# Optimization experiments

Measured on AMD Instinct MI355X. Metric: run time of the kernel, lower is better.

The kernel has to match this reference:

```python
import jax, jax.numpy as jnp
import numpy as np

# ---- static config (matches init_kwargs) ----
B, SX, SY, SZ = 1, 64, 64, 64
W = 32            # HIDDEN_DIM
L = 4             # num_fourier_layers
M1 = M2 = M3 = 8  # fourier modes per axis
PX = PY = PZ = 8  # domain padding
ALPHA = 0.05      # leaky relu slope
OUTC = 6


def conv3d(x, w, pad):
    # x: (B,C,D,H,W), w: (O,I,kd,kh,kw)
    return jax.lax.conv_general_dilated(
        x, w, window_strides=(1, 1, 1), padding=[(pad, pad)] * 3,
        dimension_numbers=('NCDHW', 'OIDHW', 'NCDHW'))


def pad1(x):
    # periodic=(0,0,0) -> zero pad 1 on every spatial side (matches ZeroPad3d chain)
    return jnp.pad(x, ((0, 0), (0, 0), (1, 1), (1, 1), (1, 1)))


def basic_block(x, w1, w2):
    # BasicBlock3D_Periodic with use_shortcut=False
    out = jax.nn.leaky_relu(conv3d(pad1(x), w1, 0), ALPHA)
    return conv3d(pad1(out), w2, 0)


def spec_apply(xft_slice, w):
    # xft_slice: complex (B,C,d1,d2,d3); w: (2C,2C,5,5,5)
    re_im = jnp.concatenate([xft_slice.real, xft_slice.imag], axis=1)  # (B,2C,...)
    out = conv3d(re_im, w, 2)                                          # (B,2C,...)
    b, c2, d1, d2, d3 = out.shape
    out = out.reshape(b, c2 // 2, 2, d1, d2, d3)
    return jax.lax.complex(out[:, :, 0], out[:, :, 1])


def spectral_conv(x, ws):
    # ws: (8, 2W, 2W, 5, 5, 5); mode-limited per-octant conv in frequency space
    b, c, n, m, l = x.shape
    xft = jnp.fft.rfftn(x, axes=(-3, -2, -1))  # (b,c,n,m,l//2+1) complex
    out = jnp.zeros((b, c, n, m, l // 2 + 1), dtype=xft.dtype)
    octs = [
        (slice(None, M1),  slice(None, M2)),
        (slice(n - M1, None), slice(None, M2)),
        (slice(None, M1),  slice(m - M2, None)),
        (slice(n - M1, None), slice(m - M2, None)),
        (slice(M1, n - M1), slice(None, M2)),
        (slice(None, M1),  slice(M2, m - M2)),
        (slice(M1, n - M1), slice(m - M2, None)),
        (slice(n - M1, None), slice(M2, m - M2)),
    ]
    for i, (s1, s2) in enumerate(octs):
        out = out.at[:, :, s1, s2, :M3].set(spec_apply(xft[:, :, s1, s2, :M3], ws[i]))
    return jnp.fft.irfftn(out, s=(n, m, l), axes=(-3, -2, -1))


def setup_inputs() -> dict:
    key = jax.random.key(0)
    ks = jax.random.split(key, 16)
    f32 = jnp.float32
    d = {
        'yeex': jax.random.normal(ks[0], (B, SX, SY, SZ), f32),
        'yeey': jax.random.normal(ks[1], (B, SX, SY, SZ), f32),
        'yeez': jax.random.normal(ks[2], (B, SX, SY, SZ), f32),
        'fc0_w': jax.random.normal(ks[3], (6, W), f32) * 0.1,
        'fc0_b': jax.random.normal(ks[4], (W,), f32) * 0.01,
        'spec_w': jax.random.normal(ks[5], (L, 8, 2 * W, 2 * W, 5, 5, 5), f32) * 0.02,
        'blk_w1': jax.random.normal(ks[6], (L, W, W, 3, 3, 3), f32) * 0.05,
        'blk_w2': jax.random.normal(ks[7], (L, W, W, 3, 3, 3), f32) * 0.05,
        'fc1_w': jax.random.normal(ks[8], (W, 128), f32) * 0.05,
        'fc1_b': jax.random.normal(ks[9], (128,), f32) * 0.01,
        'fc2_w': jax.random.normal(ks[10], (128, OUTC), f32) * 0.05,
        'fc2_b': jax.random.normal(ks[11], (OUTC,), f32) * 0.01,
    }
    return d


def reference(yeex, yeey, yeez, fc0_w, fc0_b, spec_w, blk_w1, blk_w2,
              fc1_w, fc1_b, fc2_w, fc2_b):
    b, sx, sy, sz = yeez.shape
    # normalized coordinate grid (3 channels), as in standard FNO get_grid
    gx = jnp.broadcast_to(jnp.linspace(0., 1., sx, dtype=yeex.dtype)[None, :, None, None], (b, sx, sy, sz))
    gy = jnp.broadcast_to(jnp.linspace(0., 1., sy, dtype=yeex.dtype)[None, None, :, None], (b, sx, sy, sz))
    gz = jnp.broadcast_to(jnp.linspace(0., 1., sz, dtype=yeex.dtype)[None, None, None, :], (b, sx, sy, sz))
    inp = jnp.stack([yeex, yeey, yeez, gx, gy, gz], axis=-1)  # (b,sx,sy,sz,6)

    x = inp @ fc0_w + fc0_b                      # lift: (b,sx,sy,sz,W)
    x = jnp.transpose(x, (0, 4, 1, 2, 3))        # (b,W,sx,sy,sz)
    x = jnp.pad(x, ((0, 0), (0, 0), (0, PX), (0, PY), (0, PZ)))

    for i in range(L):
        x1 = spectral_conv(x, spec_w[i])
        x2 = basic_block(x, blk_w1[i], blk_w2[i])
        x = x1 + x2 + x
        if i < L - 1:
            x = jax.nn.leaky_relu(x, ALPHA)

    x = x[:, :, :sx, :sy, :sz]                   # crop domain padding
    x = jnp.transpose(x, (0, 2, 3, 4, 1))        # (b,sx,sy,sz,W)
    x = jax.nn.leaky_relu(x @ fc1_w + fc1_b, ALPHA)
    return x @ fc2_w + fc2_b                     # (b,sx,sy,sz,OUTC)
```

## Files before the change

kernel.cpp:

```cpp
#include <hip/hip_runtime.h>
#include <math.h>

#define NS 72
#define NS2 (NS*NS)
#define NS3 (NS*NS*NS)
#define MZ 8
#define LALPHA 0.05f
#define CSCALE (1.0f/256.0f)

typedef _Float16 f16x8 __attribute__((ext_vector_type(8)));
typedef _Float16 f16x4 __attribute__((ext_vector_type(4)));
typedef float f32x4 __attribute__((ext_vector_type(4)));

__device__ __forceinline__ float leakyf(float v){ return v > 0.f ? v : LALPHA*v; }

__constant__ int c_RX0[8] = {0,64,0,64, 8,0,8,64};
__constant__ int c_RNX[8] = {8,8,8,8, 56,8,56,8};
__constant__ int c_RY0[8] = {0,0,64,64, 0,8,64,8};
__constant__ int c_RNY[8] = {8,8,8,8, 8,56,8,56};
__constant__ int c_Bbase[8] = {0,1728,3456,5184, 6912,15552,24192,32832};
__constant__ int c_BY[8]    = {12,12,12,12, 12,60,12,60};

__global__ void k_tw(float2* tw){
  int t = threadIdx.x;
  if (t < NS){
    double th = (2.0*M_PI/72.0)*(double)t;
    tw[t] = make_float2((float)cos(th), (float)sin(th));
  }
}

__global__ void k_fc0(const float* __restrict__ yx, const float* __restrict__ yy,
                      const float* __restrict__ yz, const float* __restrict__ w,
                      const float* __restrict__ b, float* __restrict__ X){
  int idx = blockIdx.x*256 + threadIdx.x;
  int z = idx % NS; int t = idx / NS; int y = t % NS; t /= NS; int x = t % NS; int c = t / NS;
  float v = 0.f;
  if (x < 64 && y < 64 && z < 64){
    int p = (x*64 + y)*64 + z;
    float i0 = yx[p], i1 = yy[p], i2 = yz[p];
    float gx = (float)x*(1.f/63.f), gy = (float)y*(1.f/63.f), gz = (float)z*(1.f/63.f);
    v = b[c] + i0*w[0*32+c] + i1*w[1*32+c] + i2*w[2*32+c]
             + gx*w[3*32+c] + gy*w[4*32+c] + gz*w[5*32+c];
  }
  X[idx] = v;
}

__global__ void k_zdft(const float* __restrict__ X, float2* __restrict__ A, const float2* __restrict__ tw){
  __shared__ float2 stw[NS];
  int tid = threadIdx.x;
  if (tid < NS) stw[tid] = tw[tid];
  __syncthreads();
  int f = blockIdx.x*256 + tid;
  const float* row = X + (size_t)f*NS;
  float ar[MZ], ai[MZ]; int tk[MZ];
  #pragma unroll
  for (int k=0;k<MZ;k++){ ar[k]=0.f; ai[k]=0.f; tk[k]=0; }
  for (int z4=0; z4<NS; z4+=4){
    float4 v4 = *(const float4*)(row + z4);
    float vs[4] = {v4.x, v4.y, v4.z, v4.w};
    #pragma unroll
    for (int zz=0; zz<4; zz++){
      float v = vs[zz];
      #pragma unroll
      for (int k=0;k<MZ;k++){
        float2 w = stw[tk[k]];
        ar[k] += v*w.x;
        ai[k] -= v*w.y;
        tk[k] += k; if (tk[k] >= NS) tk[k] -= NS;
      }
    }
  }
  float2* o = A + (size_t)f*MZ;
  #pragma unroll
  for (int k=0;k<MZ;k++) o[k] = make_float2(ar[k], ai[k]);
}

__global__ void k_ydft(const float2* __restrict__ A, float2* __restrict__ B, const float2* __restrict__ tw){
  __shared__ float2 stw[NS];
  int tid = threadIdx.x;
  if (tid < NS) stw[tid] = tw[tid];
  __syncthreads();
  int f = blockIdx.x*256 + tid;
  int ky = f % NS; int cx = f / NS;
  const float2* in = A + (size_t)cx*NS*MZ;
  float ar[MZ], ai[MZ];
  #pragma unroll
  for (int k=0;k<MZ;k++){ ar[k]=0.f; ai[k]=0.f; }
  int t = 0;
  for (int y=0;y<NS;y++){
    float2 w = stw[t]; t += ky; if (t>=NS) t-=NS;
    const float2* iy = in + y*MZ;
    #pragma unroll
    for (int k=0;k<MZ;k++){
      float2 v = iy[k];
      ar[k] += v.x*w.x + v.y*w.y;
      ai[k] += v.y*w.x - v.x*w.y;
    }
  }
  float2* o = B + (size_t)f*MZ;
  #pragma unroll
  for (int k=0;k<MZ;k++) o[k] = make_float2(ar[k], ai[k]);
}

__global__ void k_xdftL(const float2* __restrict__ B, float2* __restrict__ C, const float2* __restrict__ tw){
  __shared__ float2 stw[NS];
  int tid = threadIdx.x;
  if (tid < NS) stw[tid] = tw[tid];
  __syncthreads();
  int t = blockIdx.x*256 + tid;
  int h = t & 1; int t2 = t >> 1;
  int c = t2 >> 11; int l = t2 & 2047;
  int kx, ky;
  if (l < 576){ ky = l & 7; kx = l >> 3; }
  else if (l < 1152){ int e = l - 576; ky = 64 + (e & 7); kx = e >> 3; }
  else { int e = l - 1152; int kyi = e >> 4; int kxi = e & 15;
         ky = 8 + kyi; kx = (kxi < 8) ? kxi : 56 + kxi; }
  int k0 = h*4;
  const float2* in = B + ((size_t)c*NS2 + ky)*MZ + k0;
  float ar[4], ai[4];
  #pragma unroll
  for (int k=0;k<4;k++){ ar[k]=0.f; ai[k]=0.f; }
  int tt = 0;
  for (int x=0;x<NS;x++){
    float2 w = stw[tt]; tt += kx; if (tt>=NS) tt-=NS;
    const float2* ix = in + (size_t)x*NS*MZ;
    #pragma unroll
    for (int k=0;k<4;k++){
      float2 v = ix[k];
      ar[k] += v.x*w.x + v.y*w.y;
      ai[k] += v.y*w.x - v.x*w.y;
    }
  }
  float2* o = C + (((size_t)c*NS + kx)*NS + ky)*MZ + k0;
  #pragma unroll
  for (int k=0;k<4;k++) o[k] = make_float2(ar[k], ai[k]);
}

__global__ void k_wpackh(const float* __restrict__ W, _Float16* __restrict__ Ah){
  int e = blockIdx.x*256 + threadIdx.x;
  int i = e & 63; int o = (e>>6) & 63;
  int t2 = e >> 12; int tap = t2 % 125; int r = t2 / 125;
  const float* wr = W + (size_t)r*64*64*125;
  Ah[e] = (_Float16)wr[((size_t)(o*64 + (i&1)*32 + (i>>1)))*125 + tap];
}

__global__ void k_cpackh(const float2* __restrict__ C, _Float16* __restrict__ Bg){
  int g = blockIdx.x*256 + threadIdx.x;
  int ci = g & 31; int elem = g >> 5;
  int r = 0;
  #pragma unroll
  for (int k=1;k<8;k++) if (elem >= c_Bbase[k]) r = k;
  int el = elem - c_Bbase[r];
  int BY = c_BY[r];
  int q3 = el % 12; int tt = el / 12; int q2 = tt % BY; int q1 = tt / BY;
  int kxr = q1-2, kyr = q2-2, kzr = q3-2;
  float2 v = make_float2(0.f,0.f);
  if ((unsigned)kxr < (unsigned)c_RNX[r] && (unsigned)kyr < (unsigned)c_RNY[r] && (unsigned)kzr < 8u){
    v = C[(((size_t)ci*NS + (c_RX0[r]+kxr))*NS + (c_RY0[r]+kyr))*MZ + kzr];
  }
  _Float16* o = Bg + (size_t)elem*64 + 2*ci;
  o[0] = (_Float16)(v.x*CSCALE);
  o[1] = (_Float16)(v.y*CSCALE);
}

__global__ __launch_bounds__(64) void k_freqmfma(const _Float16* __restrict__ Ah,
                                                 const _Float16* __restrict__ Bg,
                                                 float* __restrict__ Pp){
  int gb = blockIdx.x;
  int ks = gb >> 8; int b = gb & 255;
  int r, til;
  if (b < 32){ r = b>>3; til = b&7; }
  else       { r = 4 + (b-32)/56; til = (b-32)%56; }
  int BY = c_BY[r];
  int q1, q2base;
  if (r==5 || r==7){ q1 = 2 + til/7; q2base = 2 + (til%7)*8; }
  else             { q1 = 2 + til;   q2base = 2; }
  int lane = threadIdx.x;
  int l15 = lane & 15, kg = lane >> 4;
  int q2l = q2base + (l15>>3), q3l = 2 + (l15&7);
  const _Float16* Ar = Ah + (size_t)r*125*4096;
  const _Float16* Br = Bg + (size_t)c_Bbase[r]*64;
  int lb = q2l*12 + q3l;
  f32x4 acc[4][4];
  f32x4 zz = {0.f,0.f,0.f,0.f};
  #pragma unroll
  for (int m=0;m<4;m++)
    #pragma unroll
    for (int n=0;n<4;n++) acc[m][n] = zz;
  int t0 = ks*16;
  int t1 = t0+16 < 125 ? t0+16 : 125;
  for (int tt=t0; tt<t1; tt++){
    int td = tt/25; int rm = tt - td*25; int th = rm/5; int tz = rm - th*5;
    const _Float16* At = Ar + tt*4096;
    f16x8 a[4][2];
    #pragma unroll
    for (int mt=0;mt<4;mt++){
      a[mt][0] = *(const f16x8*)(At + (mt*16+l15)*64 + kg*8);
      a[mt][1] = *(const f16x8*)(At + (mt*16+l15)*64 + 32 + kg*8);
    }
    int ebase = (q1 + td - 2)*BY*12 + lb + (th-2)*12 + (tz-2);
    f16x8 bf[4][2];
    #pragma unroll
    for (int nt=0;nt<4;nt++){
      const _Float16* bp = Br + (size_t)(ebase + nt*24)*64 + kg*8;
      bf[nt][0] = *(const f16x8*)(bp);
      bf[nt][1] = *(const f16x8*)(bp + 32);
    }
    #pragma unroll
    for (int mt=0;mt<4;mt++)
      #pragma unroll
      for (int nt=0;nt<4;nt++){
        acc[mt][nt] = __builtin_amdgcn_mfma_f32_16x16x32_f16(a[mt][0], bf[nt][0], acc[mt][nt],0,0,0);
        acc[mt][nt] = __builtin_amdgcn_mfma_f32_16x16x32_f16(a[mt][1], bf[nt][1], acc[mt][nt],0,0,0);
      }
  }
  float* base = Pp + (((size_t)ks*256 + b)*64 + lane)*64;
  #pragma unroll
  for (int mt=0;mt<4;mt++)
    #pragma unroll
    for (int nt=0;nt<4;nt++)
      *(f32x4*)(base + mt*16 + nt*4) = acc[mt][nt];
}

__global__ void k_fred(const float* __restrict__ Pp, float* __restrict__ Df){
  int t = blockIdx.x*256 + threadIdx.x;
  int mtnt = t & 15; int lane = (t>>4) & 63; int b = t >> 10;
  int mt = mtnt >> 2, nt = mtnt & 3;
  int r, til;
  if (b < 32){ r = b>>3; til = b&7; }
  else       { r = 4 + (b-32)/56; til = (b-32)%56; }
  int x0 = c_RX0[r], y0 = c_RY0[r];
  int q1, q2base;
  if (r==5 || r==7){ q1 = 2 + til/7; q2base = 2 + (til%7)*8; }
  else             { q1 = 2 + til;   q2base = 2; }
  int l15 = lane & 15, kg = lane >> 4;
  int q2l = q2base + (l15>>3), q3l = 2 + (l15&7);
  f32x4 s = {0.f,0.f,0.f,0.f};
  #pragma unroll
  for (int ks=0;ks<8;ks++){
    s += *(const f32x4*)(Pp + (((size_t)ks*256 + b)*64 + lane)*64 + mtnt*4);
  }
  int kx = x0 + q1 - 2;
  int kz = q3l - 2;
  int ky = y0 + q2l + nt*2 - 2;
  #pragma unroll
  for (int rg=0;rg<4;rg++){
    int o = mt*16 + kg*4 + rg;
    int co = o >> 1, reim = o & 1;
    Df[((((size_t)co*NS + kx)*NS + ky)*MZ + kz)*2 + reim] = s[rg]*256.0f;
  }
}

__global__ void k_invx(const float2* __restrict__ D, float2* __restrict__ E, const float2* __restrict__ tw){
  __shared__ float2 stw[NS];
  int tid = threadIdx.x;
  if (tid < NS) stw[tid] = tw[tid];
  __syncthreads();
  int f = blockIdx.x*256 + tid;
  int ky = f / 2304; int rem = f - ky*2304;
  int c = rem / NS; int x = rem - c*NS;
  const float2* in = D + ((size_t)c*NS2 + ky)*MZ;
  float ar[MZ], ai[MZ];
  #pragma unroll
  for (int k=0;k<MZ;k++){ ar[k]=0.f; ai[k]=0.f; }
  if (ky >= 8 && ky < 64){
    int t = 0;
    for (int kx=0;kx<8;kx++){
      float2 w = stw[t]; t += x; if (t>=NS) t-=NS;
      const float2* ix = in + (size_t)kx*NS*MZ;
      #pragma unroll
      for (int k=0;k<MZ;k++){
        float2 v = ix[k];
        ar[k] += v.x*w.x - v.y*w.y;
        ai[k] += v.x*w.y + v.y*w.x;
      }
    }
    t = (64*x) % NS;
    for (int kx=64;kx<NS;kx++){
      float2 w = stw[t]; t += x; if (t>=NS) t-=NS;
      const float2* ix = in + (size_t)kx*NS*MZ;
      #pragma unroll
      for (int k=0;k<MZ;k++){
        float2 v = ix[k];
        ar[k] += v.x*w.x - v.y*w.y;
        ai[k] += v.x*w.y + v.y*w.x;
      }
    }
  } else {
    int t = 0;
    for (int kx=0;kx<NS;kx++){
      float2 w = stw[t]; t += x; if (t>=NS) t-=NS;
      const float2* ix = in + (size_t)kx*NS*MZ;
      #pragma unroll
      for (int k=0;k<MZ;k++){
        float2 v = ix[k];
        ar[k] += v.x*w.x - v.y*w.y;
        ai[k] += v.x*w.y + v.y*w.x;
      }
    }
  }
  float2* o = E + (((size_t)c*NS + x)*NS + ky)*MZ;
  #pragma unroll
  for (int k=0;k<MZ;k++) o[k] = make_float2(ar[k]*(1.f/72.f), ai[k]*(1.f/72.f));
}

__global__ void k_invyz(const float2* __restrict__ E, _Float16* __restrict__ X1h, const float2* __restrict__ tw){
  __shared__ float2 stw[NS];
  int tid = threadIdx.x;
  if (tid < NS) stw[tid] = tw[tid];
  __syncthreads();
  int f = blockIdx.x*256 + tid;
  int y = f % NS; int t2 = f / NS; int x = t2 % NS; int c = t2 / NS;
  const float2* in = E + ((size_t)c*NS + x)*NS*MZ;
  float ar[MZ], ai[MZ];
  #pragma unroll
  for (int k=0;k<MZ;k++){ ar[k]=0.f; ai[k]=0.f; }
  int t = 0;
  for (int ky=0;ky<NS;ky++){
    float2 w = stw[t]; t += y; if (t>=NS) t-=NS;
    const float2* ik = in + ky*MZ;
    #pragma unroll
    for (int k=0;k<MZ;k++){
      float2 v = ik[k];
      ar[k] += v.x*w.x - v.y*w.y;
      ai[k] += v.x*w.y + v.y*w.x;
    }
  }
  const float scale = 1.f/(72.f*72.f);
  _Float16* o = X1h + (size_t)f*NS;
  int tk[MZ];
  #pragma unroll
  for (int k=0;k<MZ;k++) tk[k]=0;
  for (int z4=0; z4<NS; z4+=4){
    f16x4 hv;
    #pragma unroll
    for (int zz=0; zz<4; zz++){
      float acc = ar[0];
      #pragma unroll
      for (int k=1;k<MZ;k++){
        float2 w = stw[tk[k]];
        acc += 2.f*(ar[k]*w.x - ai[k]*w.y);
        tk[k] += k; if (tk[k] >= NS) tk[k] -= NS;
      }
      hv[zz] = (_Float16)(acc*scale);
    }
    *(f16x4*)(o + z4) = hv;
  }
}


__global__ void k_wcvt2(const float* __restrict__ w1, const float* __restrict__ w2,
                        _Float16* __restrict__ WhA, _Float16* __restrict__ WhB){
  int e = blockIdx.x*256 + threadIdx.x;
  int h = e >= 27648; int e2 = e - (h ? 27648 : 0);
  int tap = e2 >> 10; int co = (e2>>5)&31; int ci = e2&31;
  const float* w = h ? w2 : w1;
  _Float16* o = h ? WhB : WhA;
  o[e2] = (_Float16)w[(co*32+ci)*27 + tap];
}

__global__ void k_cvt16(const float* __restrict__ Xf, _Float16* __restrict__ Xg){
  int b = blockIdx.x;
  int tid = threadIdx.x;
  if (b >= 1458){
    _Float16* g = (b==1458) ? (Xg - 4096) : (Xg + (size_t)NS3*32);
    f16x8 zz = {0,0,0,0,0,0,0,0};
    f16x8* gp = (f16x8*)g;
    gp[tid] = zz; gp[tid+256] = zz;
    return;
  }
  int p = b*256 + tid;
  f16x8 o0,o1,o2,o3;
  #pragma unroll
  for (int c=0;c<8;c++){
    o0[c] = (_Float16)Xf[(size_t)c*NS3 + p];
    o1[c] = (_Float16)Xf[(size_t)(c+8)*NS3 + p];
    o2[c] = (_Float16)Xf[(size_t)(c+16)*NS3 + p];
    o3[c] = (_Float16)Xf[(size_t)(c+24)*NS3 + p];
  }
  f16x8* op = (f16x8*)(Xg + (size_t)p*32);
  op[0]=o0; op[1]=o1; op[2]=o2; op[3]=o3;
}

__global__ void k_zgH(_Float16* __restrict__ Hg){
  int e = blockIdx.x*256 + threadIdx.x;
  _Float16* g = (e < 512) ? (Hg - 4096 + e*8)
                          : (Hg + (size_t)NS3*32 + (size_t)(e-512)*8);
  f16x8 zz = {0,0,0,0,0,0,0,0};
  *(f16x8*)g = zz;
}

__global__ __launch_bounds__(256) void k_convm(const _Float16* __restrict__ Xg,
    const _Float16* __restrict__ Wh, float* __restrict__ OUT, _Float16* __restrict__ OUTH,
    const _Float16* __restrict__ X1h, const _Float16* __restrict__ XresH,
    int mode2, int do_leaky){
  int tid = threadIdx.x;
  int orig = blockIdx.x;
  int xcd = orig & 7, loc = orig >> 3;
  int wg = (xcd < 2 ? xcd*183 : 366 + (xcd-2)*182) + loc;
  int j = wg*4 + (tid>>6);
  int slab = j/81, nb = j - slab*81;
  int q0 = nb*64;
  int lane = tid & 63;
  int l15 = lane & 15, kg = lane >> 4;
  f32x4 acc[2][4];
  f32x4 zz = {0.f,0.f,0.f,0.f};
  #pragma unroll
  for (int a=0;a<2;a++)
    #pragma unroll
    for (int b=0;b<4;b++) acc[a][b] = zz;
  for (int dx=0; dx<3; dx++){
    int xx = slab + dx - 1;
    if ((unsigned)xx >= 72u) continue;
    const _Float16* Xrow = Xg + ((size_t)xx*5184 + q0)*32;
    #pragma unroll
    for (int t9=0; t9<9; t9++){
      int tap = dx*9 + t9;
      int off = ((t9/3)-1)*72 + (t9%3) - 1;
      f16x8 a0 = *(const f16x8*)(Wh + ((tap*32 + l15)*32 + kg*8));
      f16x8 a1 = *(const f16x8*)(Wh + ((tap*32 + 16 + l15)*32 + kg*8));
      const _Float16* bbase = Xrow + (off + l15)*32 + kg*8;
      f16x8 b0 = *(const f16x8*)(bbase);
      f16x8 b1 = *(const f16x8*)(bbase + 512);
      f16x8 b2 = *(const f16x8*)(bbase + 1024);
      f16x8 b3 = *(const f16x8*)(bbase + 1536);
      acc[0][0] = __builtin_amdgcn_mfma_f32_16x16x32_f16(a0,b0,acc[0][0],0,0,0);
      acc[0][1] = __builtin_amdgcn_mfma_f32_16x16x32_f16(a0,b1,acc[0][1],0,0,0);
      acc[0][2] = __builtin_amdgcn_mfma_f32_16x16x32_f16(a0,b2,acc[0][2],0,0,0);
      acc[0][3] = __builtin_amdgcn_mfma_f32_16x16x32_f16(a0,b3,acc[0][3],0,0,0);
      acc[1][0] = __builtin_amdgcn_mfma_f32_16x16x32_f16(a1,b0,acc[1][0],0,0,0);
      acc[1][1] = __builtin_amdgcn_mfma_f32_16x16x32_f16(a1,b1,acc[1][1],0,0,0);
      acc[1][2] = __builtin_amdgcn_mfma_f32_16x16x32_f16(a1,b2,acc[1][2],0,0,0);
      acc[1][3] = __builtin_amdgcn_mfma_f32_16x16x32_f16(a1,b3,acc[1][3],0,0,0);
    }
  }
  if (mode2){
    #pragma unroll
    for (int nt=0; nt<4; nt++){
      int q = q0 + nt*16 + l15;
      int y = q/72, z = q - y*72;
      bool edge = (y==0)||(y==71)||(z==0)||(z==71);
      #pragma unroll
      for (int c2=0;c2<2;c2++){
        #pragma unroll
        for (int r=0;r<4;r++){
          int co = c2*16 + kg*4 + r;
          size_t idx = (size_t)co*NS3 + (size_t)slab*5184 + q;
          float v = acc[c2][nt][r];
          if (!edge){
            v += (float)X1h[idx] + (float)XresH[((size_t)slab*5184 + q)*32 + co];
            if (do_leaky) v = leakyf(v);
          }
          OUT[idx] = v;
        }
      }
    }
  } else {
    #pragma unroll
    for (int nt=0; nt<4; nt++){
      int q = q0 + nt*16 + l15;
      int y = q/72, z = q - y*72;
      bool edge = (y==0)||(y==71)||(z==0)||(z==71);
      _Float16* hp = OUTH + ((size_t)slab*5184 + q)*32 + kg*4;
      #pragma unroll
      for (int c2=0;c2<2;c2++){
        f32x4 av = acc[c2][nt];
        f16x4 hv;
        #pragma unroll
        for (int r=0;r<4;r++){
          float v = av[r];
          if (!edge) v = leakyf(v);
          hv[r] = (_Float16)v;
        }
        *(f16x4*)(hp + c2*16) = hv;
      }
    }
  }
}

__global__ void k_corrH(_Float16* __restrict__ H, const _Float16* __restrict__ Xg,
                        const _Float16* __restrict__ Wh){
  int t = blockIdx.x*256 + threadIdx.x;
  int co = t & 31; int t2 = t >> 5;
  int e = t2 % 284; int x = t2 / 284;
  int y, z;
  if (e < 72){ y = 0; z = e; }
  else if (e < 144){ y = 71; z = e - 72; }
  else if (e < 214){ z = 0; y = e - 143; }
  else { z = 71; y = e - 213; }
  int q = y*72 + z;
  float corr = 0.f;
  for (int tap=0; tap<27; tap++){
    int dx = tap/9, rr = tap%9, dy = rr/3, dz = rr%3;
    int xx = x + dx - 1;
    if ((unsigned)xx >= 72u) continue;
    int yy = y + dy - 1, zz = z + dz - 1;
    if ((unsigned)yy < 72u && (unsigned)zz < 72u) continue;
    int lin = (xx*5184 + q + (dy-1)*72 + (dz-1))*32;
    const _Float16* V = Xg + lin;
    const _Float16* Wr = Wh + (tap*32 + co)*32;
    float s = 0.f;
    #pragma unroll
    for (int ci=0; ci<32; ci++) s += (float)V[ci]*(float)Wr[ci];
    corr += s;
  }
  size_t idx = ((size_t)x*5184 + q)*32 + co;
  float v = (float)H[idx] - corr;
  v = leakyf(v);
  H[idx] = (_Float16)v;
}

__global__ void k_corr(float* __restrict__ OUT, const _Float16* __restrict__ Xg,
                       const _Float16* __restrict__ Wh, const _Float16* __restrict__ X1h,
                       const _Float16* __restrict__ XresH, int mode2, int do_leaky){
  int t = blockIdx.x*256 + threadIdx.x;
  int co = t & 31; int t2 = t >> 5;
  int e = t2 % 284; int x = t2 / 284;
  int y, z;
  if (e < 72){ y = 0; z = e; }
  else if (e < 144){ y = 71; z = e - 72; }
  else if (e < 214){ z = 0; y = e - 143; }
  else { z = 71; y = e - 213; }
  int q = y*72 + z;
  float corr = 0.f;
  for (int tap=0; tap<27; tap++){
    int dx = tap/9, rr = tap%9, dy = rr/3, dz = rr%3;
    int xx = x + dx - 1;
    if ((unsigned)xx >= 72u) continue;
    int yy = y + dy - 1, zz = z + dz - 1;
    if ((unsigned)yy < 72u && (unsigned)zz < 72u) continue;
    int lin = (xx*5184 + q + (dy-1)*72 + (dz-1))*32;
    const _Float16* V = Xg + lin;
    const _Float16* Wr = Wh + (tap*32 + co)*32;
    float s = 0.f;
    #pragma unroll
    for (int ci=0; ci<32; ci++) s += (float)V[ci]*(float)Wr[ci];
    corr += s;
  }
  size_t idx = (size_t)co*NS3 + (size_t)x*5184 + q;
  float v = OUT[idx] - corr;
  if (mode2) v += (float)X1h[idx] + (float)XresH[((size_t)x*5184 + q)*32 + co];
  if (do_leaky) v = leakyf(v);
  OUT[idx] = v;
}

__global__ void k_head(const float* __restrict__ X, const float* __restrict__ w1, const float* __restrict__ b1,
                       const float* __restrict__ w2, const float* __restrict__ b2, float* __restrict__ out){
  __shared__ float s1t[32*128];
  __shared__ float sb1[128];
  __shared__ float s2[128*6];
  __shared__ float sb2[6];
  int tid = threadIdx.x;
  for (int e=tid;e<4096;e+=256){ int j=e>>5, c=e&31; s1t[e]=w1[c*128+j]; }
  if (tid<128) sb1[tid]=b1[tid];
  for (int e=tid;e<768;e+=256) s2[e]=w2[e];
  if (tid<6) sb2[tid]=b2[tid];
  __syncthreads();
  int p0 = blockIdx.x*256 + tid;
  float xin[2][32];
  float acc[2][6];
  #pragma unroll
  for (int vv=0; vv<2; vv++){
    int p = p0 + vv*131072;
    int z = p % 64; int t = p / 64; int y = t % 64; int x = t / 64;
    size_t q = ((size_t)x*NS + y)*NS + z;
    #pragma unroll
    for (int c=0;c<32;c++) xin[vv][c] = X[(size_t)c*NS3 + q];
    #pragma unroll
    for (int o=0;o<6;o++) acc[vv][o]=sb2[o];
  }
  for (int j=0;j<128;j++){
    const float4* wj = (const float4*)(s1t + j*32);
    float h0 = sb1[j], h1 = h0;
    #pragma unroll
    for (int c4=0;c4<8;c4++){
      float4 w = wj[c4];
      h0 += xin[0][c4*4+0]*w.x + xin[0][c4*4+1]*w.y + xin[0][c4*4+2]*w.z + xin[0][c4*4+3]*w.w;
      h1 += xin[1][c4*4+0]*w.x + xin[1][c4*4+1]*w.y + xin[1][c4*4+2]*w.z + xin[1][c4*4+3]*w.w;
    }
    h0 = leakyf(h0); h1 = leakyf(h1);
    const float* s2j = s2 + j*6;
    #pragma unroll
    for (int o=0;o<6;o++){
      float wv = s2j[o];
      acc[0][o] += h0*wv;
      acc[1][o] += h1*wv;
    }
  }
  #pragma unroll
  for (int vv=0; vv<2; vv++){
    float* O = out + (size_t)(p0 + vv*131072)*6;
    #pragma unroll
    for (int o=0;o<6;o++) O[o]=acc[vv][o];
  }
}

extern "C" void kernel_launch(void* const* d_in, const int* in_sizes, int n_in,
                              void* d_out, int out_size, void* d_ws, size_t ws_size,
                              hipStream_t stream) {
  const float* yeex = (const float*)d_in[0];
  const float* yeey = (const float*)d_in[1];
  const float* yeez = (const float*)d_in[2];
  const float* fc0w = (const float*)d_in[3];
  const float* fc0b = (const float*)d_in[4];
  const float* specw= (const float*)d_in[5];
  const float* bw1  = (const float*)d_in[6];
  const float* bw2  = (const float*)d_in[7];
  const float* fc1w = (const float*)d_in[8];
  const float* fc1b = (const float*)d_in[9];
  const float* fc2w = (const float*)d_in[10];
  const float* fc2b = (const float*)d_in[11];
  float* out = (float*)d_out;
  float* ws  = (float*)d_ws;

  float*  P0 = ws;
  float*  X1s = ws + 11943936;
  float*  P2 = ws + 23887872;
  float2* A  = (float2*)(ws + 35831808);
  float2* B  = (float2*)(ws + 41140224);
  float2* Cf = (float2*)(ws + 46448640);
  float2* Df = (float2*)(ws + 51757056);
  float2* TW = (float2*)(ws + 57065472);
  _Float16* Ah = (_Float16*)A;
  _Float16* Bg = (_Float16*)B;
  float*    Pp = X1s;
  _Float16* X1h = (_Float16*)X1s;
  _Float16* XhG = (_Float16*)(ws + 35831808) + 4096;
  _Float16* HhG = (_Float16*)(ws + 41807872) + 4096;
  _Float16* WhA = (_Float16*)(ws + 47783936);
  _Float16* WhB = (_Float16*)(ws + 47797760);

  float* curX = P0; float* curY = P2;

  k_tw<<<1,128,0,stream>>>(TW);
  k_fc0<<<46656,256,0,stream>>>(yeex,yeey,yeez,fc0w,fc0b,curX);
  for (int i=0;i<4;i++){
    k_zdft<<<648,256,0,stream>>>(curX, A, TW);
    k_ydft<<<648,256,0,stream>>>(A, B, TW);
    k_xdftL<<<512,256,0,stream>>>(B, Cf, TW);
    k_wpackh<<<16000,256,0,stream>>>(specw + (size_t)i*8*64*64*125, Ah);
    k_cpackh<<<5184,256,0,stream>>>(Cf, Bg);
    hipMemsetAsync(Df, 0, (size_t)1327104*8, stream);
    k_freqmfma<<<2048,64,0,stream>>>(Ah, Bg, Pp);
    k_fred<<<1024,256,0,stream>>>(Pp, (float*)Df);
    k_invx<<<648,256,0,stream>>>(Df, A, TW);
    k_invyz<<<648,256,0,stream>>>(A, X1h, TW);
    k_wcvt2<<<216,256,0,stream>>>(bw1 + (size_t)i*27648, bw2 + (size_t)i*27648, WhA, WhB);
    k_cvt16<<<1460,256,0,stream>>>(curX, XhG);
    k_zgH<<<4,256,0,stream>>>(HhG);
    k_convm<<<1458,256,0,stream>>>(XhG, WhA, nullptr, HhG, nullptr, nullptr, 0, 1);
    k_corrH<<<2556,256,0,stream>>>(HhG, XhG, WhA);
    k_convm<<<1458,256,0,stream>>>(HhG, WhB, curY, nullptr, X1h, XhG, 1, (i<3)?1:0);
    k_corr<<<2556,256,0,stream>>>(curY, HhG, WhB, X1h, XhG, 1, (i<3)?1:0);
    float* tmp = curX; curX = curY; curY = tmp;
  }
  k_head<<<512,256,0,stream>>>(curX, fc1w, fc1b, fc2w, fc2b, out);
}
```

Measured before the change: 2.362 ms.

## Stage conv input rows in LDS and share across waves in k_convm

The 3x3x3 conv kernel now uses 192-thread blocks of three waves covering 192 contiguous y-z points per x-slab. For each dx plane it cooperatively copies a 338-point halo window into shared memory, then serves the nine y/z tap loads from LDS instead of global memory. The aim is to cut redundant global and L2 traffic for overlapping taps. In exchange it adds two barriers per dx plane, uses about 21 KB of LDS per block, and changes the grid and XCD mapping.

Result: faster. 2.172 ms (-8.0%).

```diff
diff --git a/kernel.cpp b/kernel.cpp
--- a/kernel.cpp
+++ b/kernel.cpp
@@ -390,17 +390,18 @@
   *(f16x8*)g = zz;
 }
 
-__global__ __launch_bounds__(256) void k_convm(const _Float16* __restrict__ Xg,
+__global__ __launch_bounds__(192) void k_convm(const _Float16* __restrict__ Xg,
     const _Float16* __restrict__ Wh, float* __restrict__ OUT, _Float16* __restrict__ OUTH,
     const _Float16* __restrict__ X1h, const _Float16* __restrict__ XresH,
     int mode2, int do_leaky){
+  __shared__ _Float16 sB[338*32];
   int tid = threadIdx.x;
   int orig = blockIdx.x;
   int xcd = orig & 7, loc = orig >> 3;
-  int wg = (xcd < 2 ? xcd*183 : 366 + (xcd-2)*182) + loc;
-  int j = wg*4 + (tid>>6);
-  int slab = j/81, nb = j - slab*81;
-  int q0 = nb*64;
+  int wg = xcd*243 + loc;
+  int slab = wg/27, tb = wg - slab*27;
+  int q0 = tb*192;
+  int wid = tid >> 6;
   int lane = tid & 63;
   int l15 = lane & 15, kg = lane >> 4;
   f32x4 acc[2][4];
@@ -409,21 +410,30 @@
   for (int a=0;a<2;a++)
     #pragma unroll
     for (int b=0;b<4;b++) acc[a][b] = zz;
+  int wbase = l15*32 + kg*8;
+  int lbase = wid*64 + 73 + l15;
   for (int dx=0; dx<3; dx++){
     int xx = slab + dx - 1;
     if ((unsigned)xx >= 72u) continue;
-    const _Float16* Xrow = Xg + ((size_t)xx*5184 + q0)*32;
+    __syncthreads();
+    {
+      const f16x8* src = (const f16x8*)(Xg + ((long long)xx*5184 + q0 - 73)*32);
+      f16x8* dst = (f16x8*)sB;
+      for (int e=tid; e<1352; e+=192) dst[e] = src[e];
+    }
+    __syncthreads();
+    const _Float16* Wdx = Wh + dx*9216;
     #pragma unroll
     for (int t9=0; t9<9; t9++){
-      int tap = dx*9 + t9;
       int off = ((t9/3)-1)*72 + (t9%3) - 1;
-      f16x8 a0 = *(const f16x8*)(Wh + ((tap*32 + l15)*32 + kg*8));
-      f16x8 a1 = *(const f16x8*)(Wh + ((tap*32 + 16 + l15)*32 + kg*8));
-      const _Float16* bbase = Xrow + (off + l15)*32 + kg*8;
-      f16x8 b0 = *(const f16x8*)(bbase);
-      f16x8 b1 = *(const f16x8*)(bbase + 512);
-      f16x8 b2 = *(const f16x8*)(bbase + 1024);
-      f16x8 b3 = *(const f16x8*)(bbase + 1536);
+      const _Float16* wp = Wdx + t9*1024 + wbase;
+      f16x8 a0 = *(const f16x8*)(wp);
+      f16x8 a1 = *(const f16x8*)(wp + 512);
+      const _Float16* bb = sB + (lbase + off)*32 + kg*8;
+      f16x8 b0 = *(const f16x8*)(bb);
+      f16x8 b1 = *(const f16x8*)(bb + 512);
+      f16x8 b2 = *(const f16x8*)(bb + 1024);
+      f16x8 b3 = *(const f16x8*)(bb + 1536);
       acc[0][0] = __builtin_amdgcn_mfma_f32_16x16x32_f16(a0,b0,acc[0][0],0,0,0);
       acc[0][1] = __builtin_amdgcn_mfma_f32_16x16x32_f16(a0,b1,acc[0][1],0,0,0);
       acc[0][2] = __builtin_amdgcn_mfma_f32_16x16x32_f16(a0,b2,acc[0][2],0,0,0);
@@ -434,10 +444,11 @@
       acc[1][3] = __builtin_amdgcn_mfma_f32_16x16x32_f16(a1,b3,acc[1][3],0,0,0);
     }
   }
+  int q0w = q0 + wid*64;
   if (mode2){
     #pragma unroll
     for (int nt=0; nt<4; nt++){
-      int q = q0 + nt*16 + l15;
+      int q = q0w + nt*16 + l15;
       int y = q/72, z = q - y*72;
       bool edge = (y==0)||(y==71)||(z==0)||(z==71);
       #pragma unroll
@@ -458,7 +469,7 @@
   } else {
     #pragma unroll
     for (int nt=0; nt<4; nt++){
-      int q = q0 + nt*16 + l15;
+      int q = q0w + nt*16 + l15;
       int y = q/72, z = q - y*72;
       bool edge = (y==0)||(y==71)||(z==0)||(z==71);
       _Float16* hp = OUTH + ((size_t)slab*5184 + q)*32 + kg*4;
@@ -648,9 +659,9 @@
     k_wcvt2<<<216,256,0,stream>>>(bw1 + (size_t)i*27648, bw2 + (size_t)i*27648, WhA, WhB);
     k_cvt16<<<1460,256,0,stream>>>(curX, XhG);
     k_zgH<<<4,256,0,stream>>>(HhG);
-    k_convm<<<1458,256,0,stream>>>(XhG, WhA, nullptr, HhG, nullptr, nullptr, 0, 1);
+    k_convm<<<1944,192,0,stream>>>(XhG, WhA, nullptr, HhG, nullptr, nullptr, 0, 1);
     k_corrH<<<2556,256,0,stream>>>(HhG, XhG, WhA);
-    k_convm<<<1458,256,0,stream>>>(HhG, WhB, curY, nullptr, X1h, XhG, 1, (i<3)?1:0);
+    k_convm<<<1944,192,0,stream>>>(HhG, WhB, curY, nullptr, X1h, XhG, 1, (i<3)?1:0);
     k_corr<<<2556,256,0,stream>>>(curY, HhG, WhB, X1h, XhG, 1, (i<3)?1:0);
     float* tmp = curX; curX = curY; curY = tmp;
   }
```
